# Optimization experiments

Measured on AMD Instinct MI355X. Metric: run time of the kernel, lower is better.

Reference implementation:

```python
import jax, jax.numpy as jnp
import numpy as np
import math

D_MODEL = 1024
D_STATE = 16
D_CONV = 4
EXPAND = 2
D_INNER = EXPAND * D_MODEL
BATCH = 8
SEQ_LEN = 2048
DT_MIN, DT_MAX = 1e-3, 1e-1


def setup_inputs() -> dict:
    key = jax.random.key(0)
    ks = jax.random.split(key, 8)
    scale = 0.02
    x = jax.random.normal(ks[0], (BATCH, SEQ_LEN, D_MODEL), dtype=jnp.float32)
    W_in = jax.random.normal(ks[1], (2 * D_INNER, D_MODEL), dtype=jnp.float32) * scale
    conv_w = jax.random.normal(ks[2], (D_INNER, 1, D_CONV), dtype=jnp.float32) * scale  # depthwise [O,I/g,K]
    conv_b = jnp.zeros((D_INNER,), dtype=jnp.float32)
    W_x = jax.random.normal(ks[3], (2 * D_STATE + 1, D_INNER), dtype=jnp.float32) * scale
    W_dt = jax.random.normal(ks[4], (D_INNER, 1), dtype=jnp.float32) * scale
    # dt bias init: softplus^{-1}(dt) with dt ~ LogUniform(dt_min, dt_max)
    u = jax.random.uniform(ks[5], (D_INNER,), dtype=jnp.float32)
    dt = jnp.clip(jnp.exp(u * (math.log(DT_MAX) - math.log(DT_MIN)) + math.log(DT_MIN)), DT_MIN, None)
    b_dt = dt + jnp.log(-jnp.expm1(-dt))
    # A_log = log(A), A[d,n] = n+1
    A_log = jnp.log(jnp.broadcast_to(jnp.arange(1, D_STATE + 1, dtype=jnp.float32), (D_INNER, D_STATE)))
    D = jnp.ones((D_INNER,), dtype=jnp.float32)
    W_out = jax.random.normal(ks[6], (D_MODEL, D_INNER), dtype=jnp.float32) * scale
    return {"x": x, "W_in": W_in, "conv_w": conv_w, "conv_b": conv_b,
            "W_x": W_x, "W_dt": W_dt, "b_dt": b_dt, "A_log": A_log, "D": D, "W_out": W_out}


def _selective_ssm(xs, W_x, W_dt, b_dt, A_log, D):
    # xs: [B, L, Di]
    B_, L, Di = xs.shape
    N = A_log.shape[1]
    A = -jnp.exp(A_log)  # [Di, N]
    x_dbl = xs @ W_x.T  # [B, L, 2N+1]
    dt_raw, Bm, Cm = jnp.split(x_dbl, [1, 1 + N], axis=-1)
    dt = jax.nn.softplus(dt_raw @ W_dt.T + b_dt)  # [B, L, Di]

    def step(h, inp):
        dt_t, B_t, C_t, x_t = inp  # [B,Di], [B,N], [B,N], [B,Di]
        A_bar = jnp.exp(dt_t[..., None] * A)                      # [B, Di, N]
        h = A_bar * h + (dt_t * x_t)[..., None] * B_t[:, None, :]  # [B, Di, N]
        y_t = jnp.einsum('bdn,bn->bd', h, C_t)
        return h, y_t

    h0 = jnp.zeros((B_, Di, N), dtype=xs.dtype)
    inps = (jnp.moveaxis(dt, 1, 0), jnp.moveaxis(Bm, 1, 0),
            jnp.moveaxis(Cm, 1, 0), jnp.moveaxis(xs, 1, 0))
    _, ys = jax.lax.scan(step, h0, inps)  # ys: [L, B, Di]
    return jnp.moveaxis(ys, 0, 1) + D * xs


def reference(x, W_in, conv_w, conv_b, W_x, W_dt, b_dt, A_log, D, W_out):
    B_, L, _ = x.shape
    xz = x @ W_in.T  # [B, L, 2*Di]
    xi, z = jnp.split(xz, 2, axis=-1)
    # causal depthwise conv1d (torch pads both sides by d_conv-1 then slices [:L] == left pad)
    xc = jnp.transpose(xi, (0, 2, 1))  # [B, Di, L]
    xc = jax.lax.conv_general_dilated(
        xc, conv_w, window_strides=(1,), padding=[(conv_w.shape[-1] - 1, 0)],
        dimension_numbers=('NCH', 'OIH', 'NCH'), feature_group_count=conv_w.shape[0])
    xc = xc + conv_b[None, :, None]
    xs = jax.nn.silu(jnp.transpose(xc, (0, 2, 1)))  # [B, L, Di]
    y = _selective_ssm(xs, W_x, W_dt, b_dt, A_log, D)
    out = (y * jax.nn.silu(z)) @ W_out.T  # [B, L, d_model]
    return out
```

## Files before the change

### kernel.cpp

```cpp
#include <hip/hip_runtime.h>
#include <math.h>

#define BB    8
#define LL    2048
#define DMOD  1024
#define DI    2048
#define NST   16
#define MR    (BB*LL)
#define NCH   16
#define CLEN  128
#define XDW   36

typedef unsigned short bf16_t;
typedef __attribute__((ext_vector_type(8))) __bf16 bf16x8;
typedef __attribute__((ext_vector_type(4))) float  f32x4;

__device__ __forceinline__ float b2f(bf16_t u) {
  return __uint_as_float(((unsigned int)u) << 16);
}
__device__ __forceinline__ bf16_t f2bn(float f) {
  __bf16 h = (__bf16)f;
  return *(bf16_t*)&h;
}

__device__ __forceinline__ void cstore(float* p, float v)  { *p = v; }
__device__ __forceinline__ void cstore(bf16_t* p, float v) { *p = f2bn(v); }

__device__ __forceinline__ void gld16(const bf16_t* g, bf16_t* l) {
  __builtin_amdgcn_global_load_lds(
      (const __attribute__((address_space(1))) unsigned int*)g,
      (__attribute__((address_space(3))) unsigned int*)l, 16, 0, 0);
}

__device__ __forceinline__ float softplus(float x) {
  return (x > 20.f) ? x : __logf(1.f + __expf(x));
}
__device__ __forceinline__ float silu(float z) {
  return z * __builtin_amdgcn_rcpf(1.f + __expf(-z));
}

__global__ __launch_bounds__(256) void cvt_bf16(
    const float* __restrict__ in, bf16_t* __restrict__ out, int n4)
{
  int i = blockIdx.x * 256 + threadIdx.x;
  if (i >= n4) return;
  float4 v = ((const float4*)in)[i];
  ushort4 u;
  u.x = f2bn(v.x); u.y = f2bn(v.y); u.z = f2bn(v.z); u.w = f2bn(v.w);
  ((ushort4*)out)[i] = u;
}

__global__ __launch_bounds__(256) void cvt_wx(
    const float* __restrict__ W_x, bf16_t* __restrict__ Wx_bf)
{
  int i = blockIdx.x * 256 + threadIdx.x;
  int j = i >> 11;
  Wx_bf[i] = (j < 33) ? f2bn(W_x[i]) : (bf16_t)0;
}

template <typename TC>
__global__ __launch_bounds__(256) void mgemm_nt(
    const bf16_t* __restrict__ A, const bf16_t* __restrict__ B,
    TC* __restrict__ C, int N, int K)
{
  __shared__ __align__(16) bf16_t As[128 * 32];
  __shared__ __align__(16) bf16_t Bs[128 * 32];
  const int tid  = threadIdx.x;
  const int wave = tid >> 6;
  const int lane = tid & 63;

  const int nbx  = N >> 7;
  const int lg   = 31 - __clz(nbx);
  const int nwg  = (int)(gridDim.x * gridDim.y);
  const int flat = (int)(blockIdx.y * gridDim.x + blockIdx.x);
  const int swz  = (flat & 7) * (nwg >> 3) + (flat >> 3);
  const int m0 = (swz >> lg) * 128;
  const int n0 = (swz & (nbx - 1)) * 128;

  const int wm = (wave >> 1) * 64;
  const int wn = (wave & 1) * 64;
  const int fr = lane & 15;
  const int quad = lane >> 4;

  const int srow = wave * 32 + (lane >> 2);
  const int scol = (lane & 3) * 8;
  const bf16_t* Ag0 = A + (size_t)(m0 + srow) * K + scol;
  const bf16_t* Ag1 = Ag0 + (size_t)16 * K;
  const bf16_t* Bg0 = B + (size_t)(n0 + srow) * K + scol;
  const bf16_t* Bg1 = Bg0 + (size_t)16 * K;
  bf16_t* lA0 = As + (wave * 32) * 32;
  bf16_t* lA1 = As + (wave * 32 + 16) * 32;
  bf16_t* lB0 = Bs + (wave * 32) * 32;
  bf16_t* lB1 = Bs + (wave * 32 + 16) * 32;

  f32x4 acc[4][4];
#pragma unroll
  for (int i = 0; i < 4; ++i)
#pragma unroll
    for (int j = 0; j < 4; ++j) acc[i][j] = (f32x4){0.f, 0.f, 0.f, 0.f};

  for (int k0 = 0; k0 < K; k0 += 32) {
    __syncthreads();
    gld16(Ag0 + k0, lA0);
    gld16(Ag1 + k0, lA1);
    gld16(Bg0 + k0, lB0);
    gld16(Bg1 + k0, lB1);
    __syncthreads();

    bf16x8 a[4], b[4];
#pragma unroll
    for (int i = 0; i < 4; ++i)
      a[i] = *(const bf16x8*)&As[(wm + i * 16 + fr) * 32 + quad * 8];
#pragma unroll
    for (int j = 0; j < 4; ++j)
      b[j] = *(const bf16x8*)&Bs[(wn + j * 16 + fr) * 32 + quad * 8];
#pragma unroll
    for (int i = 0; i < 4; ++i)
#pragma unroll
      for (int j = 0; j < 4; ++j)
        acc[i][j] = __builtin_amdgcn_mfma_f32_16x16x32_bf16(a[i], b[j], acc[i][j], 0, 0, 0);
  }

#pragma unroll
  for (int i = 0; i < 4; ++i)
#pragma unroll
    for (int j = 0; j < 4; ++j) {
#pragma unroll
      for (int r = 0; r < 4; ++r) {
        int grow = m0 + wm + i * 16 + quad * 4 + r;
        int gcol = n0 + wn + j * 16 + fr;
        cstore(&C[(size_t)grow * N + gcol], acc[i][j][r]);
      }
    }
}

__global__ __launch_bounds__(256) void xdbl_mfma(
    const bf16_t* __restrict__ xs, const bf16_t* __restrict__ Wx_bf,
    float* __restrict__ xdbl)
{
  __shared__ __align__(16) bf16_t As[2 * 64 * 32];
  __shared__ __align__(16) bf16_t Bs[2 * 64 * 32];
  const int tid  = threadIdx.x;
  const int wave = tid >> 6;
  const int lane = tid & 63;
  const int m0 = blockIdx.x * 64;
  const int fr = lane & 15;
  const int quad = lane >> 4;

  const int srow = wave * 16 + (lane >> 2);
  const int scol = (lane & 3) * 8;
  const bf16_t* Ag = xs + (size_t)(m0 + srow) * DI + scol;
  const bf16_t* Bg = Wx_bf + (size_t)srow * DI + scol;
  bf16_t* lA = As + wave * 512;
  bf16_t* lB = Bs + wave * 512;

  f32x4 acc[3];
#pragma unroll
  for (int jt = 0; jt < 3; ++jt) acc[jt] = (f32x4){0.f, 0.f, 0.f, 0.f};

  for (int k0 = 0; k0 < DI; k0 += 64) {
    __syncthreads();
#pragma unroll
    for (int kk = 0; kk < 2; ++kk) {
      gld16(Ag + k0 + kk * 32, lA + kk * 2048);
      gld16(Bg + k0 + kk * 32, lB + kk * 2048);
    }
    __syncthreads();

#pragma unroll
    for (int kk = 0; kk < 2; ++kk) {
      bf16x8 a = *(const bf16x8*)&As[kk * 2048 + (wave * 16 + fr) * 32 + quad * 8];
#pragma unroll
      for (int jt = 0; jt < 3; ++jt) {
        bf16x8 b = *(const bf16x8*)&Bs[kk * 2048 + (jt * 16 + fr) * 32 + quad * 8];
        acc[jt] = __builtin_amdgcn_mfma_f32_16x16x32_bf16(a, b, acc[jt], 0, 0, 0);
      }
    }
  }

#pragma unroll
  for (int jt = 0; jt < 3; ++jt) {
#pragma unroll
    for (int r = 0; r < 4; ++r) {
      int grow = m0 + wave * 16 + quad * 4 + r;
      int j = jt * 16 + fr;
      if (j < 33) {
        int col = (j == 0) ? 0 : (j + 3);
        xdbl[(size_t)grow * XDW + col] = acc[jt][r];
      }
    }
  }
}

__global__ __launch_bounds__(256) void conv_silu(
    const bf16_t* __restrict__ xz, const float* __restrict__ cw,
    const float* __restrict__ cb, bf16_t* __restrict__ xs)
{
  int idx = blockIdx.x * 256 + threadIdx.x;
  int d4 = idx & 511;
  int l  = (idx >> 9) & 2047;
  int b  = idx >> 20;
  int d  = d4 * 4;

  float wch[4][4];
#pragma unroll
  for (int c = 0; c < 4; ++c)
#pragma unroll
    for (int k = 0; k < 4; ++k) wch[c][k] = cw[(d + c) * 4 + k];

  float acc0 = cb[d+0], acc1 = cb[d+1], acc2 = cb[d+2], acc3 = cb[d+3];
  size_t rowbase = ((size_t)b * LL + l) * 4096 + d;
#pragma unroll
  for (int k = 0; k < 4; ++k) {
    if (l - 3 + k >= 0) {
      ushort4 u = *(const ushort4*)(xz + rowbase - (size_t)(3 - k) * 4096);
      acc0 += b2f(u.x) * wch[0][k];
      acc1 += b2f(u.y) * wch[1][k];
      acc2 += b2f(u.z) * wch[2][k];
      acc3 += b2f(u.w) * wch[3][k];
    }
  }
  ushort4 o;
  o.x = f2bn(silu(acc0)); o.y = f2bn(silu(acc1));
  o.z = f2bn(silu(acc2)); o.w = f2bn(silu(acc3));
  *(ushort4*)(xs + ((size_t)b * LL + l) * (size_t)DI + d) = o;
}

__global__ __launch_bounds__(256) void scan_pass1(
    const float* __restrict__ xdbl, const bf16_t* __restrict__ xs,
    const float* __restrict__ W_dt, const float* __restrict__ b_dt,
    const float* __restrict__ A_log, float* __restrict__ states)
{
  const int bid = blockIdx.x;
  const int dg = bid & 7, c = (bid >> 3) & 15, b = bid >> 7;
  const int d = dg * 256 + threadIdx.x;

  const float A2_0 = -__expf(A_log[(size_t)d * NST]) * 1.44269504f;
  bool ok = true;
#pragma unroll
  for (int n = 1; n < NST; ++n) {
    float a = -__expf(A_log[(size_t)d * NST + n]) * 1.44269504f;
    ok = ok && (fabsf(a - (float)(n + 1) * A2_0) <= 1e-3f * (float)(n + 1));
  }
  __shared__ int s_ok;
  __shared__ float sx[64 * XDW];
  if (threadIdx.x == 0) s_ok = 1;
  __syncthreads();
  if (!ok) s_ok = 0;
  __syncthreads();
  const bool fast = (s_ok != 0);

  float h[NST];
#pragma unroll
  for (int n = 0; n < NST; ++n) h[n] = 0.f;
  const float wdt = W_dt[d], bdt = b_dt[d];
  float dts = 0.f;
  const size_t rbase = (size_t)b * LL + c * CLEN;
  float xv = b2f(xs[rbase * DI + d]);

  if (fast) {
    for (int s = 0; s < CLEN; s += 64) {
      __syncthreads();
      const float* xg = xdbl + (rbase + s) * XDW;
      for (int q = threadIdx.x; q < 64 * XDW; q += 256) sx[q] = xg[q];
      __syncthreads();
#pragma unroll 2
      for (int u = 0; u < 64; ++u) {
        int tn = s + u + 1;
        float nx = 0.f;
        if (tn < CLEN) nx = b2f(xs[(rbase + tn) * DI + d]);
        float dtr = sx[u * XDW];
        float dt = softplus(fmaf(dtr, wdt, bdt));
        dts += dt;
        float dx = dt * xv;
        float wv[NST];
        wv[0] = exp2f(dt * A2_0);
#pragma unroll
        for (int n = 1; n < NST; ++n)
          wv[n] = wv[(n - 1) >> 1] * wv[n - 1 - ((n - 1) >> 1)];
        const float4* Bp = (const float4*)&sx[u * XDW + 4];
#pragma unroll
        for (int n4 = 0; n4 < 4; ++n4) {
          float4 Bv = Bp[n4];
          float bb[4] = {Bv.x, Bv.y, Bv.z, Bv.w};
#pragma unroll
          for (int k = 0; k < 4; ++k) {
            int n = n4 * 4 + k;
            h[n] = fmaf(wv[n], h[n], dx * bb[k]);
          }
        }
        xv = nx;
      }
    }
    size_t sb = (((size_t)b * NCH + c) * DI + d) * 32;
    float Wv[NST];
    Wv[0] = exp2f(dts * A2_0);
#pragma unroll
    for (int n = 1; n < NST; ++n)
      Wv[n] = Wv[(n - 1) >> 1] * Wv[n - 1 - ((n - 1) >> 1)];
#pragma unroll
    for (int n = 0; n < NST; ++n) {
      states[sb + n]      = Wv[n];
      states[sb + 16 + n] = h[n];
    }
  } else {
    float A2[NST];
#pragma unroll
    for (int n = 0; n < NST; ++n)
      A2[n] = -__expf(A_log[(size_t)d * NST + n]) * 1.44269504f;
    for (int s = 0; s < CLEN; s += 64) {
      __syncthreads();
      const float* xg = xdbl + (rbase + s) * XDW;
      for (int q = threadIdx.x; q < 64 * XDW; q += 256) sx[q] = xg[q];
      __syncthreads();
#pragma unroll 2
      for (int u = 0; u < 64; ++u) {
        int tn = s + u + 1;
        float nx = 0.f;
        if (tn < CLEN) nx = b2f(xs[(rbase + tn) * DI + d]);
        float dtr = sx[u * XDW];
        float dt = softplus(fmaf(dtr, wdt, bdt));
        dts += dt;
        float dx = dt * xv;
        const float4* Bp = (const float4*)&sx[u * XDW + 4];
#pragma unroll
        for (int n4 = 0; n4 < 4; ++n4) {
          float4 Bv = Bp[n4];
          float bb[4] = {Bv.x, Bv.y, Bv.z, Bv.w};
#pragma unroll
          for (int k = 0; k < 4; ++k) {
            int n = n4 * 4 + k;
            h[n] = fmaf(exp2f(dt * A2[n]), h[n], dx * bb[k]);
          }
        }
        xv = nx;
      }
    }
    size_t sb = (((size_t)b * NCH + c) * DI + d) * 32;
#pragma unroll
    for (int n = 0; n < NST; ++n) {
      states[sb + n]      = exp2f(dts * A2[n]);
      states[sb + 16 + n] = h[n];
    }
  }
}

__global__ __launch_bounds__(256) void scan_pass2(float* __restrict__ states)
{
  int t = blockIdx.x * 256 + threadIdx.x;
  int n = t & 15, d = (t >> 4) & 2047, b = t >> 15;
  float h = 0.f;
  for (int c = 0; c < NCH; ++c) {
    size_t sb = (((size_t)b * NCH + c) * DI + d) * 32;
    float P  = states[sb + n];
    float h0 = states[sb + 16 + n];
    states[sb + n] = h;
    h = fmaf(P, h, h0);
  }
}

__global__ __launch_bounds__(256) void scan_pass3(
    const float* __restrict__ xdbl, const bf16_t* __restrict__ xz,
    bf16_t* __restrict__ xs, const float* __restrict__ states,
    const float* __restrict__ W_dt, const float* __restrict__ b_dt,
    const float* __restrict__ A_log, const float* __restrict__ Dp)
{
  const int bid = blockIdx.x;
  const int dg = bid & 7, c = (bid >> 3) & 15, b = bid >> 7;
  const int d = dg * 256 + threadIdx.x;

  const float A2_0 = -__expf(A_log[(size_t)d * NST]) * 1.44269504f;
  bool ok = true;
#pragma unroll
  for (int n = 1; n < NST; ++n) {
    float a = -__expf(A_log[(size_t)d * NST + n]) * 1.44269504f;
    ok = ok && (fabsf(a - (float)(n + 1) * A2_0) <= 1e-3f * (float)(n + 1));
  }
  __shared__ int s_ok;
  __shared__ float sx[64 * XDW];
  if (threadIdx.x == 0) s_ok = 1;
  __syncthreads();
  if (!ok) s_ok = 0;
  __syncthreads();
  const bool fast = (s_ok != 0);

  float h[NST];
  size_t sb = (((size_t)b * NCH + c) * DI + d) * 32;
#pragma unroll
  for (int n = 0; n < NST; ++n) h[n] = states[sb + n];
  const float wdt = W_dt[d], bdt = b_dt[d];
  const float Dd = Dp[d];
  const size_t rbase = (size_t)b * LL + c * CLEN;

  float xv = b2f(xs[rbase * DI + d]);
  float zv = b2f(xz[rbase * 4096 + DI + d]);

  if (fast) {
    for (int s = 0; s < CLEN; s += 64) {
      __syncthreads();
      const float* xg = xdbl + (rbase + s) * XDW;
      for (int q = threadIdx.x; q < 64 * XDW; q += 256) sx[q] = xg[q];
      __syncthreads();
#pragma unroll 2
      for (int u = 0; u < 64; ++u) {
        size_t r = rbase + s + u;
        int tn = s + u + 1;
        float nx = 0.f, nz = 0.f;
        if (tn < CLEN) {
          nx = b2f(xs[(rbase + tn) * DI + d]);
          nz = b2f(xz[(rbase + tn) * 4096 + DI + d]);
        }
        float dtr = sx[u * XDW];
        float dt = softplus(fmaf(dtr, wdt, bdt));
        float dx = dt * xv;
        float y = Dd * xv;
        float wv[NST];
        wv[0] = exp2f(dt * A2_0);
#pragma unroll
        for (int n = 1; n < NST; ++n)
          wv[n] = wv[(n - 1) >> 1] * wv[n - 1 - ((n - 1) >> 1)];
        const float4* Bp = (const float4*)&sx[u * XDW + 4];
        const float4* Cp = (const float4*)&sx[u * XDW + 20];
#pragma unroll
        for (int n4 = 0; n4 < 4; ++n4) {
          float4 Bv = Bp[n4];
          float4 Cv = Cp[n4];
          float bb[4] = {Bv.x, Bv.y, Bv.z, Bv.w};
          float cc[4] = {Cv.x, Cv.y, Cv.z, Cv.w};
#pragma unroll
          for (int k = 0; k < 4; ++k) {
            int n = n4 * 4 + k;
            h[n] = fmaf(wv[n], h[n], dx * bb[k]);
            y = fmaf(h[n], cc[k], y);
          }
        }
        xs[r * DI + d] = f2bn(y * silu(zv));
        xv = nx; zv = nz;
      }
    }
  } else {
    float A2[NST];
#pragma unroll
    for (int n = 0; n < NST; ++n)
      A2[n] = -__expf(A_log[(size_t)d * NST + n]) * 1.44269504f;
    for (int s = 0; s < CLEN; s += 64) {
      __syncthreads();
      const float* xg = xdbl + (rbase + s) * XDW;
      for (int q = threadIdx.x; q < 64 * XDW; q += 256) sx[q] = xg[q];
      __syncthreads();
#pragma unroll 2
      for (int u = 0; u < 64; ++u) {
        size_t r = rbase + s + u;
        int tn = s + u + 1;
        float nx = 0.f, nz = 0.f;
        if (tn < CLEN) {
          nx = b2f(xs[(rbase + tn) * DI + d]);
          nz = b2f(xz[(rbase + tn) * 4096 + DI + d]);
        }
        float dtr = sx[u * XDW];
        float dt = softplus(fmaf(dtr, wdt, bdt));
        float dx = dt * xv;
        float y = Dd * xv;
        const float4* Bp = (const float4*)&sx[u * XDW + 4];
        const float4* Cp = (const float4*)&sx[u * XDW + 20];
#pragma unroll
        for (int n4 = 0; n4 < 4; ++n4) {
          float4 Bv = Bp[n4];
          float4 Cv = Cp[n4];
          float bb[4] = {Bv.x, Bv.y, Bv.z, Bv.w};
          float cc[4] = {Cv.x, Cv.y, Cv.z, Cv.w};
#pragma unroll
          for (int k = 0; k < 4; ++k) {
            int n = n4 * 4 + k;
            h[n] = fmaf(exp2f(dt * A2[n]), h[n], dx * bb[k]);
            y = fmaf(h[n], cc[k], y);
          }
        }
        xs[r * DI + d] = f2bn(y * silu(zv));
        xv = nx; zv = nz;
      }
    }
  }
}

extern "C" void kernel_launch(void* const* d_in, const int* in_sizes, int n_in,
                              void* d_out, int out_size, void* d_ws, size_t ws_size,
                              hipStream_t stream)
{
  const float* x     = (const float*)d_in[0];
  const float* W_in  = (const float*)d_in[1];
  const float* cw    = (const float*)d_in[2];
  const float* cb    = (const float*)d_in[3];
  const float* W_x   = (const float*)d_in[4];
  const float* W_dt  = (const float*)d_in[5];
  const float* b_dt  = (const float*)d_in[6];
  const float* A_log = (const float*)d_in[7];
  const float* Dp    = (const float*)d_in[8];
  const float* W_out = (const float*)d_in[9];
  float* out = (float*)d_out;

  bf16_t* xz = (bf16_t*)d_ws;
  bf16_t* xs = xz + (size_t)MR * 4096;

  bf16_t* x_bf    = (bf16_t*)d_out;
  bf16_t* Win_bf  = x_bf + (size_t)MR * DMOD;
  bf16_t* Wx_bf   = Win_bf + (size_t)4096 * DMOD;
  float*  states  = (float*)d_out;
  float*  xdbl    = states + (size_t)BB * NCH * DI * 32;
  bf16_t* Wout_bf = xz;

  cvt_bf16<<<(MR*DMOD/4 + 255)/256, 256, 0, stream>>>(x, x_bf, MR*DMOD/4);
  cvt_bf16<<<(4096*DMOD/4 + 255)/256, 256, 0, stream>>>(W_in, Win_bf, 4096*DMOD/4);
  cvt_wx<<<(64*DI)/256, 256, 0, stream>>>(W_x, Wx_bf);
  mgemm_nt<bf16_t><<<dim3(4096/128, MR/128), 256, 0, stream>>>(x_bf, Win_bf, xz, 4096, DMOD);
  conv_silu<<<(BB*LL*512)/256, 256, 0, stream>>>(xz, cw, cb, xs);
  xdbl_mfma<<<MR/64, 256, 0, stream>>>(xs, Wx_bf, xdbl);
  scan_pass1<<<BB*NCH*8, 256, 0, stream>>>(xdbl, xs, W_dt, b_dt, A_log, states);
  scan_pass2<<<(BB*DI*NST)/256, 256, 0, stream>>>(states);
  scan_pass3<<<BB*NCH*8, 256, 0, stream>>>(xdbl, xz, xs, states, W_dt, b_dt, A_log, Dp);
  cvt_bf16<<<(DMOD*DI/4 + 255)/256, 256, 0, stream>>>(W_out, Wout_bf, DMOD*DI/4);
  mgemm_nt<float><<<dim3(DMOD/128, MR/128), 256, 0, stream>>>(xs, Wout_bf, out, DMOD, DI);
}
```

Baseline: 732.9 us.

## Rewrite GEMM as 256x256-tile, triple-buffered, swizzled-LDS MFMA kernel

Replaces the 128x128 single-buffered GEMM with a 512-thread kernel computing 256x256 tiles. It uses a three-stage LDS ring with direct global-to-LDS loads issued two k-steps ahead, so there is one barrier per k-step. The LDS column chunks are XOR-swizzled to avoid bank conflicts, and s_setprio is raised around the MFMA block. This targets global-load latency and LDS stalls in both projection GEMMs. In exchange it drops the block-index swizzle, launches fewer blocks, and raises per-thread accumulator register pressure.

```diff
diff --git a/kernel.cpp b/kernel.cpp
--- a/kernel.cpp
+++ b/kernel.cpp
@@ -59,70 +59,91 @@
 }
 
 template <typename TC>
-__global__ __launch_bounds__(256) void mgemm_nt(
+__global__ __launch_bounds__(512) void mgemm_big(
     const bf16_t* __restrict__ A, const bf16_t* __restrict__ B,
     TC* __restrict__ C, int N, int K)
 {
-  __shared__ __align__(16) bf16_t As[128 * 32];
-  __shared__ __align__(16) bf16_t Bs[128 * 32];
+  __shared__ __align__(16) bf16_t As[3][256 * 32];
+  __shared__ __align__(16) bf16_t Bs[3][256 * 32];
   const int tid  = threadIdx.x;
   const int wave = tid >> 6;
   const int lane = tid & 63;
-
-  const int nbx  = N >> 7;
-  const int lg   = 31 - __clz(nbx);
-  const int nwg  = (int)(gridDim.x * gridDim.y);
-  const int flat = (int)(blockIdx.y * gridDim.x + blockIdx.x);
-  const int swz  = (flat & 7) * (nwg >> 3) + (flat >> 3);
-  const int m0 = (swz >> lg) * 128;
-  const int n0 = (swz & (nbx - 1)) * 128;
-
-  const int wm = (wave >> 1) * 64;
-  const int wn = (wave & 1) * 64;
+  const int m0 = blockIdx.y * 256;
+  const int n0 = blockIdx.x * 256;
   const int fr = lane & 15;
   const int quad = lane >> 4;
-
-  const int srow = wave * 32 + (lane >> 2);
-  const int scol = (lane & 3) * 8;
-  const bf16_t* Ag0 = A + (size_t)(m0 + srow) * K + scol;
-  const bf16_t* Ag1 = Ag0 + (size_t)16 * K;
-  const bf16_t* Bg0 = B + (size_t)(n0 + srow) * K + scol;
-  const bf16_t* Bg1 = Bg0 + (size_t)16 * K;
-  bf16_t* lA0 = As + (wave * 32) * 32;
-  bf16_t* lA1 = As + (wave * 32 + 16) * 32;
-  bf16_t* lB0 = Bs + (wave * 32) * 32;
-  bf16_t* lB1 = Bs + (wave * 32 + 16) * 32;
-
-  f32x4 acc[4][4];
-#pragma unroll
-  for (int i = 0; i < 4; ++i)
+  const int wm = (wave >> 2) * 128;
+  const int wn = (wave & 3) * 64;
+
+  const int srow = tid >> 2;
+  const int schk = tid & 3;
+  const int ssw  = schk ^ ((srow >> 1) & 3);
+  const bf16_t* Ag = A + (size_t)(m0 + srow) * K + ssw * 8;
+  const bf16_t* Bg = B + (size_t)(n0 + srow) * K + ssw * 8;
+  const size_t r128 = (size_t)128 * K;
+
+  int aoff[8], boff[4];
+#pragma unroll
+  for (int i = 0; i < 8; ++i) {
+    int row = wm + i * 16 + fr;
+    aoff[i] = row * 32 + ((quad ^ ((row >> 1) & 3)) * 8);
+  }
+#pragma unroll
+  for (int j = 0; j < 4; ++j) {
+    int row = wn + j * 16 + fr;
+    boff[j] = row * 32 + ((quad ^ ((row >> 1) & 3)) * 8);
+  }
+
+  f32x4 acc[8][4];
+#pragma unroll
+  for (int i = 0; i < 8; ++i)
 #pragma unroll
     for (int j = 0; j < 4; ++j) acc[i][j] = (f32x4){0.f, 0.f, 0.f, 0.f};
 
-  for (int k0 = 0; k0 < K; k0 += 32) {
-    __syncthreads();
-    gld16(Ag0 + k0, lA0);
-    gld16(Ag1 + k0, lA1);
-    gld16(Bg0 + k0, lB0);
-    gld16(Bg1 + k0, lB1);
-    __syncthreads();
-
-    bf16x8 a[4], b[4];
-#pragma unroll
-    for (int i = 0; i < 4; ++i)
-      a[i] = *(const bf16x8*)&As[(wm + i * 16 + fr) * 32 + quad * 8];
-#pragma unroll
-    for (int j = 0; j < 4; ++j)
-      b[j] = *(const bf16x8*)&Bs[(wn + j * 16 + fr) * 32 + quad * 8];
-#pragma unroll
-    for (int i = 0; i < 4; ++i)
+  const int nkt = K >> 5;
+  gld16(Ag,            &As[0][wave * 512]);
+  gld16(Ag + r128,     &As[0][4096 + wave * 512]);
+  gld16(Bg,            &Bs[0][wave * 512]);
+  gld16(Bg + r128,     &Bs[0][4096 + wave * 512]);
+  gld16(Ag + 32,       &As[1][wave * 512]);
+  gld16(Ag + r128 + 32,&As[1][4096 + wave * 512]);
+  gld16(Bg + 32,       &Bs[1][wave * 512]);
+  gld16(Bg + r128 + 32,&Bs[1][4096 + wave * 512]);
+  asm volatile("s_waitcnt vmcnt(4)\n\ts_barrier" ::: "memory");
+
+  for (int t = 0; t < nkt; ++t) {
+    const int p = t % 3;
+    if (t + 2 < nkt) {
+      const int p2 = (t + 2) % 3;
+      const size_t ko = (size_t)(t + 2) * 32;
+      gld16(Ag + ko,        &As[p2][wave * 512]);
+      gld16(Ag + r128 + ko, &As[p2][4096 + wave * 512]);
+      gld16(Bg + ko,        &Bs[p2][wave * 512]);
+      gld16(Bg + r128 + ko, &Bs[p2][4096 + wave * 512]);
+    }
+    const bf16_t* Ab = &As[p][0];
+    const bf16_t* Bb = &Bs[p][0];
+    bf16x8 a[8], b[4];
+#pragma unroll
+    for (int i = 0; i < 8; ++i) a[i] = *(const bf16x8*)&Ab[aoff[i]];
+#pragma unroll
+    for (int j = 0; j < 4; ++j) b[j] = *(const bf16x8*)&Bb[boff[j]];
+    __builtin_amdgcn_s_setprio(1);
+#pragma unroll
+    for (int i = 0; i < 8; ++i)
 #pragma unroll
       for (int j = 0; j < 4; ++j)
         acc[i][j] = __builtin_amdgcn_mfma_f32_16x16x32_bf16(a[i], b[j], acc[i][j], 0, 0, 0);
-  }
-
-#pragma unroll
-  for (int i = 0; i < 4; ++i)
+    __builtin_amdgcn_s_setprio(0);
+    if (t + 2 < nkt) {
+      asm volatile("s_waitcnt vmcnt(4)\n\ts_barrier" ::: "memory");
+    } else if (t + 1 < nkt) {
+      asm volatile("s_waitcnt vmcnt(0)\n\ts_barrier" ::: "memory");
+    }
+  }
+
+#pragma unroll
+  for (int i = 0; i < 8; ++i)
 #pragma unroll
     for (int j = 0; j < 4; ++j) {
 #pragma unroll
@@ -512,12 +533,12 @@
   cvt_bf16<<<(MR*DMOD/4 + 255)/256, 256, 0, stream>>>(x, x_bf, MR*DMOD/4);
   cvt_bf16<<<(4096*DMOD/4 + 255)/256, 256, 0, stream>>>(W_in, Win_bf, 4096*DMOD/4);
   cvt_wx<<<(64*DI)/256, 256, 0, stream>>>(W_x, Wx_bf);
-  mgemm_nt<bf16_t><<<dim3(4096/128, MR/128), 256, 0, stream>>>(x_bf, Win_bf, xz, 4096, DMOD);
+  mgemm_big<bf16_t><<<dim3(4096/256, MR/256), 512, 0, stream>>>(x_bf, Win_bf, xz, 4096, DMOD);
   conv_silu<<<(BB*LL*512)/256, 256, 0, stream>>>(xz, cw, cb, xs);
   xdbl_mfma<<<MR/64, 256, 0, stream>>>(xs, Wx_bf, xdbl);
   scan_pass1<<<BB*NCH*8, 256, 0, stream>>>(xdbl, xs, W_dt, b_dt, A_log, states);
   scan_pass2<<<(BB*DI*NST)/256, 256, 0, stream>>>(states);
   scan_pass3<<<BB*NCH*8, 256, 0, stream>>>(xdbl, xz, xs, states, W_dt, b_dt, A_log, Dp);
   cvt_bf16<<<(DMOD*DI/4 + 255)/256, 256, 0, stream>>>(W_out, Wout_bf, DMOD*DI/4);
-  mgemm_nt<float><<<dim3(DMOD/128, MR/128), 256, 0, stream>>>(xs, Wout_bf, out, DMOD, DI);
-}
+  mgemm_big<float><<<dim3(DMOD/256, MR/256), 512, 0, stream>>>(xs, Wout_bf, out, DMOD, DI);
+}
```

New measurement: 720.1 us. About the same (-1.7%).
